# Performance work log

Hardware: AMD Instinct MI355X
Metric: run time of the kernel (lower is better)

## Reference

```python
import jax, jax.numpy as jnp
import numpy as np

NUM_EMBEDDINGS = 1024
EMBEDDING_DIM = 256


def setup_inputs() -> dict:
    key = jax.random.key(0)
    kx, kw = jax.random.split(key)
    x = jax.random.normal(kx, (64, 32, 32, EMBEDDING_DIM), dtype=jnp.float32)
    # nn.Linear(embedding_dim, num_embeddings).weight has shape [K, D]
    W = jax.random.normal(kw, (NUM_EMBEDDINGS, EMBEDDING_DIM), dtype=jnp.float32) * (1.0 / np.sqrt(EMBEDDING_DIM))
    return {"x": x, "W": W}


def reference(x, W):
    # flatten tokens: [N, D]
    flat = x.reshape(-1, EMBEDDING_DIM)
    sim = flat @ W.T
    distances = (jnp.sum(flat * flat, axis=1, keepdims=True)
                 + jnp.sum(W * W, axis=1)
                 - 2.0 * sim)
    indices = jnp.argmin(distances, axis=1)[:, None]  # [N, 1], matches torch unsqueeze(1)
    # one-hot @ W is exactly a row gather of the codebook
    quantized = jnp.take(W, indices[:, 0], axis=0).reshape(x.shape)
    return quantized, indices
```

## Files before the change

### kernel.cpp

```cpp
#include <hip/hip_runtime.h>
#include <float.h>

typedef _Float16 half8  __attribute__((ext_vector_type(8)));
typedef __fp16   fp16x2 __attribute__((ext_vector_type(2)));
typedef float    f32x4  __attribute__((ext_vector_type(4)));

#define NTOK  65536
#define DIM   256
#define NCODE 1024
#define TT    64
#define NCT   16
#define CAP   4096
#define TAU   0.08f
#define BIAS  64.0f

__device__ inline half8 pack8(float4 a, float4 b) {
    union { half8 v; fp16x2 h[4]; } u;
    u.h[0] = __builtin_amdgcn_cvt_pkrtz(a.x, a.y);
    u.h[1] = __builtin_amdgcn_cvt_pkrtz(a.z, a.w);
    u.h[2] = __builtin_amdgcn_cvt_pkrtz(b.x, b.y);
    u.h[3] = __builtin_amdgcn_cvt_pkrtz(b.z, b.w);
    return u.v;
}
__device__ inline unsigned umn(unsigned a, unsigned b) { return a < b ? a : b; }
__device__ inline unsigned umx(unsigned a, unsigned b) { return a > b ? a : b; }

__device__ inline void gload16(const void* g, void* l) {
    __builtin_amdgcn_global_load_lds(
        (__attribute__((address_space(1))) void*)(size_t)g,
        (__attribute__((address_space(3))) void*)l,
        16, 0, 0);
}

__global__ __launch_bounds__(256) void prep_kernel(const float* __restrict__ W,
                                                   float* __restrict__ nw_out,
                                                   half8* __restrict__ wh_out) {
    const int tid = threadIdx.x;
    const int k = blockIdx.x * 8 + (tid >> 5);
    const int c = tid & 31;
    const float4* wr = (const float4*)(W + (size_t)k * DIM + c * 8);
    float4 u = wr[0], v = wr[1];
    wh_out[(size_t)k * 32 + c] = pack8(u, v);
    double a = (double)u.x * u.x + (double)u.y * u.y + (double)u.z * u.z + (double)u.w * u.w
             + (double)v.x * v.x + (double)v.y * v.y + (double)v.z * v.z + (double)v.w * v.w;
    #pragma unroll
    for (int m = 1; m <= 16; m <<= 1) a += __shfl_xor(a, m);
    if (c == 0) nw_out[k] = (float)a;
}

template <bool PRE>
__global__ __launch_bounds__(256) __attribute__((amdgpu_waves_per_eu(4, 4)))
void vq_kernel(
    const float* __restrict__ x, const float* __restrict__ W,
    const float* __restrict__ nwp, const half8* __restrict__ whp,
    float* __restrict__ outq, float* __restrict__ outidx)
{
    __shared__ _Float16 wtile[64][256];
    __shared__ float nw_s[NCODE];
    __shared__ float nx_s[TT];
    __shared__ unsigned long long best64[TT];
    __shared__ int cnt_s;
    __shared__ int bk_s[TT];
    unsigned* cand = (unsigned*)&wtile[0][0];

    const int tid = threadIdx.x, tb = blockIdx.x * TT;
    const int wv = tid >> 6, l = tid & 63;
    const int lg = l >> 4;
    const int lr = l & 15;

    if (PRE) {
        ((float4*)nw_s)[tid] = ((const float4*)nwp)[tid];
    } else {
        #pragma unroll
        for (int c = 0; c < 4; ++c) {
            const int k = (tid << 2) + c;
            const float4* wr = (const float4*)(W + (size_t)k * DIM);
            double a0 = 0.0, a1 = 0.0;
            for (int q = 0; q < DIM / 4; ++q) {
                float4 v = wr[q];
                a0 += (double)v.x * v.x + (double)v.y * v.y;
                a1 += (double)v.z * v.z + (double)v.w * v.w;
            }
            nw_s[k] = (float)(a0 + a1);
        }
    }
    if (tid == 0) cnt_s = 0;
    if (tid < TT) best64[tid] = ~0ull;

    const int trow = tb + (wv << 4) + lr;
    half8 xa[8];
    {
        double a0 = 0.0, a1 = 0.0;
        #pragma unroll
        for (int s = 0; s < 8; ++s) {
            const float4* p = (const float4*)(x + (size_t)trow * DIM + (s << 5) + (lg << 3));
            float4 u = p[0], v = p[1];
            xa[s] = pack8(u, v);
            a0 += (double)u.x * u.x + (double)u.y * u.y + (double)v.x * v.x + (double)v.y * v.y;
            a1 += (double)u.z * u.z + (double)u.w * u.w + (double)v.z * v.z + (double)v.w * v.w;
        }
        double nx = a0 + a1;
        nx += __shfl_xor(nx, 16);
        nx += __shfl_xor(nx, 32);
        if (lg == 0) nx_s[(wv << 4) + lr] = (float)nx;
    }

    unsigned srcoff[8];
    #pragma unroll
    for (int j = 0; j < 8; ++j) {
        const unsigned g = (unsigned)(j * 256 + tid);
        srcoff[j] = (g & ~31u) | ((g & 31u) ^ ((g >> 5) & 31u));
    }

    unsigned b0[4], b1[4];
    #pragma unroll
    for (int j = 0; j < 4; ++j) { b0[j] = 0xFFFFFFFFu; b1[j] = 0xFFFFFFFFu; }

    for (int ct = 0; ct < NCT; ++ct) {
        __syncthreads();
        if (PRE) {
            #pragma unroll
            for (int j = 0; j < 8; ++j)
                gload16(whp + (size_t)ct * 2048 + srcoff[j],
                        (_Float16*)&wtile[0][0] + (size_t)(j * 256 + tid) * 8);
        } else {
            const int n = tid >> 2, qq = tid & 3;
            const float4* srcp = (const float4*)(W + (size_t)(ct * 64 + n) * DIM + (qq << 6));
            #pragma unroll
            for (int i = 0; i < 8; ++i) {
                float4 a = srcp[2 * i], b = srcp[2 * i + 1];
                const int c = (qq << 3) + i, p = c ^ (n & 31);
                *(half8*)&wtile[n][p << 3] = pack8(a, b);
            }
        }
        __syncthreads();

        f32x4 acc[4];
        #pragma unroll
        for (int st = 0; st < 4; ++st)
            #pragma unroll
            for (int j = 0; j < 4; ++j) acc[st][j] = 0.0f;

        #pragma unroll
        for (int sp = 0; sp < 8; ++sp) {
            const int c = (sp << 2) + lg;
            #pragma unroll
            for (int st = 0; st < 4; ++st) {
                const int n = (st << 4) + lr;
                const int p = c ^ (n & 31);
                half8 q = *(const half8*)&wtile[n][p << 3];
                acc[st] = __builtin_amdgcn_mfma_f32_16x16x32_f16(xa[sp], q, acc[st], 0, 0, 0);
            }
        }

        #pragma unroll
        for (int st = 0; st < 4; ++st) {
            const int kk = (ct << 6) + (st << 4) + lr;
            const float nwb = nw_s[kk] + BIAS;
            #pragma unroll
            for (int j = 0; j < 4; ++j) {
                const float c = fmaf(acc[st][j], -2.0f, nwb);
                const unsigned u = (__float_as_uint(c) & 0xFFFFFC00u) | (unsigned)kk;
                const unsigned lo = umn(u, b0[j]), hi = umx(u, b0[j]);
                b0[j] = lo;
                b1[j] = umn(hi, b1[j]);
            }
        }
    }

    __syncthreads();

    #pragma unroll
    for (int j = 0; j < 4; ++j) {
        unsigned v = b0[j];
        #pragma unroll
        for (int m = 1; m <= 8; m <<= 1) v = umn(v, (unsigned)__shfl_xor((int)v, m));
        const float thr = __uint_as_float(v & 0xFFFFFC00u) + TAU;
        const int t = (wv << 4) + (lg << 2) + j;
        if (__uint_as_float(b0[j] & 0xFFFFFC00u) <= thr) {
            int i = atomicAdd(&cnt_s, 1);
            if (i < CAP) cand[i] = ((unsigned)t << 10) | (b0[j] & 1023u);
        }
        if (__uint_as_float(b1[j] & 0xFFFFFC00u) <= thr) {
            int i = atomicAdd(&cnt_s, 1);
            if (i < CAP) cand[i] = ((unsigned)t << 10) | (b1[j] & 1023u);
        }
    }
    __syncthreads();

    const int nc = min(cnt_s, CAP);
    for (int c = wv; c < nc; c += 4) {
        const unsigned en = cand[c];
        const int t = en >> 10, k = en & 1023;
        float4 xv = ((const float4*)(x + (size_t)(tb + t) * DIM))[l];
        float4 wr = ((const float4*)(W + (size_t)k * DIM))[l];
        float s = fmaf(xv.x, wr.x, fmaf(xv.y, wr.y, fmaf(xv.z, wr.z, xv.w * wr.w)));
        #pragma unroll
        for (int m = 1; m <= 32; m <<= 1) s += __shfl_xor(s, m);
        const float dv = (nx_s[t] + nw_s[k]) - 2.0f * s;
        if (l == 0) {
            unsigned long long key = ((unsigned long long)__float_as_uint(dv) << 32) | (unsigned)k;
            atomicMin(&best64[t], key);
        }
    }
    __syncthreads();

    if (tid < TT) {
        const int bk = (int)(best64[tid] & 1023u);
        bk_s[tid] = bk;
        outidx[tb + tid] = (float)bk;
    }
    __syncthreads();

    for (int i = tid; i < TT * (DIM / 4); i += 256) {
        const int t = i >> 6, j = i & 63;
        const float4* wr = (const float4*)(W + (size_t)bk_s[t] * DIM);
        ((float4*)(outq + (size_t)(tb + t) * DIM))[j] = wr[j];
    }
}

extern "C" void kernel_launch(void* const* d_in, const int* in_sizes, int n_in,
                              void* d_out, int out_size, void* d_ws, size_t ws_size,
                              hipStream_t stream) {
    const float* x = (const float*)d_in[0];
    const float* W = (const float*)d_in[1];
    float* outq   = (float*)d_out;
    float* outidx = outq + (size_t)NTOK * DIM;

    const size_t need = 4096 + (size_t)NCODE * DIM * sizeof(_Float16);
    if (ws_size >= need) {
        float* nw_ws = (float*)d_ws;
        half8* wh_ws = (half8*)((char*)d_ws + 4096);
        prep_kernel<<<NCODE / 8, 256, 0, stream>>>(W, nw_ws, wh_ws);
        vq_kernel<true><<<NTOK / TT, 256, 0, stream>>>(x, W, nw_ws, wh_ws, outq, outidx);
    } else {
        vq_kernel<false><<<NTOK / TT, 256, 0, stream>>>(x, W, nullptr, nullptr, outq, outidx);
    }
}
```

Baseline: 159.3 us.

## Retile waves into 2x2 token-by-code MFMA blocks with shared threshold reduction

Each wave now computes two 16-token tiles against two 16-code subtiles of the shared codebook tile, instead of one token tile against four code subtiles. This halves the LDS fragment reads per MFMA, because each codebook fragment is reused across two token fragments. Each wave now sees only half of each code tile, so the per-token minimum is combined across the two code-group waves with shared-memory atomicMin before candidates are thresholded. In exchange, each x row is loaded from global memory by two waves, the x register footprint doubles, and an extra reduction pass and barrier are added.

```diff
diff --git a/kernel.cpp b/kernel.cpp
--- a/kernel.cpp
+++ b/kernel.cpp
@@ -58,6 +58,7 @@
     __shared__ _Float16 wtile[64][256];
     __shared__ float nw_s[NCODE];
     __shared__ float nx_s[TT];
+    __shared__ unsigned tmin_s[TT];
     __shared__ unsigned long long best64[TT];
     __shared__ int cnt_s;
     __shared__ int bk_s[TT];
@@ -67,6 +68,8 @@
     const int wv = tid >> 6, l = tid & 63;
     const int lg = l >> 4;
     const int lr = l & 15;
+    const int tg = wv & 1;
+    const int cg = wv >> 1;
 
     if (PRE) {
         ((float4*)nw_s)[tid] = ((const float4*)nwp)[tid];
@@ -85,44 +88,53 @@
         }
     }
     if (tid == 0) cnt_s = 0;
-    if (tid < TT) best64[tid] = ~0ull;
-
-    const int trow = tb + (wv << 4) + lr;
-    half8 xa[8];
+    if (tid < TT) { best64[tid] = ~0ull; tmin_s[tid] = 0xFFFFFFFFu; }
+
+    half8 xa0[8], xa1[8];
     {
-        double a0 = 0.0, a1 = 0.0;
-        #pragma unroll
-        for (int s = 0; s < 8; ++s) {
-            const float4* p = (const float4*)(x + (size_t)trow * DIM + (s << 5) + (lg << 3));
-            float4 u = p[0], v = p[1];
-            xa[s] = pack8(u, v);
-            a0 += (double)u.x * u.x + (double)u.y * u.y + (double)v.x * v.x + (double)v.y * v.y;
-            a1 += (double)u.z * u.z + (double)u.w * u.w + (double)v.z * v.z + (double)v.w * v.w;
-        }
-        double nx = a0 + a1;
-        nx += __shfl_xor(nx, 16);
-        nx += __shfl_xor(nx, 32);
-        if (lg == 0) nx_s[(wv << 4) + lr] = (float)nx;
-    }
-
-    unsigned srcoff[8];
-    #pragma unroll
-    for (int j = 0; j < 8; ++j) {
-        const unsigned g = (unsigned)(j * 256 + tid);
-        srcoff[j] = (g & ~31u) | ((g & 31u) ^ ((g >> 5) & 31u));
-    }
-
-    unsigned b0[4], b1[4];
-    #pragma unroll
-    for (int j = 0; j < 4; ++j) { b0[j] = 0xFFFFFFFFu; b1[j] = 0xFFFFFFFFu; }
+        const float4* p0 = (const float4*)(x + (size_t)(tb + (tg << 5) + lr) * DIM + (lg << 3));
+        const float4* p1 = (const float4*)(x + (size_t)(tb + (tg << 5) + 16 + lr) * DIM + (lg << 3));
+        double a0 = 0.0, a1 = 0.0, c0 = 0.0, c1 = 0.0;
+        #pragma unroll
+        for (int sp = 0; sp < 8; ++sp) {
+            float4 u = p0[sp * 8], v = p0[sp * 8 + 1];
+            xa0[sp] = pack8(u, v);
+            float4 uu = p1[sp * 8], vv = p1[sp * 8 + 1];
+            xa1[sp] = pack8(uu, vv);
+            if (cg == 0) {
+                a0 += (double)u.x * u.x + (double)u.y * u.y + (double)v.x * v.x + (double)v.y * v.y;
+                a1 += (double)u.z * u.z + (double)u.w * u.w + (double)v.z * v.z + (double)v.w * v.w;
+                c0 += (double)uu.x * uu.x + (double)uu.y * uu.y + (double)vv.x * vv.x + (double)vv.y * vv.y;
+                c1 += (double)uu.z * uu.z + (double)uu.w * uu.w + (double)vv.z * vv.z + (double)vv.w * vv.w;
+            }
+        }
+        if (cg == 0) {
+            double n0 = a0 + a1, n1 = c0 + c1;
+            n0 += __shfl_xor(n0, 16); n0 += __shfl_xor(n0, 32);
+            n1 += __shfl_xor(n1, 16); n1 += __shfl_xor(n1, 32);
+            if (lg == 0) {
+                nx_s[(tg << 5) + lr]      = (float)n0;
+                nx_s[(tg << 5) + 16 + lr] = (float)n1;
+            }
+        }
+    }
+
+    unsigned b0[2][4], b1[2][4];
+    #pragma unroll
+    for (int s = 0; s < 2; ++s)
+        #pragma unroll
+        for (int j = 0; j < 4; ++j) { b0[s][j] = 0xFFFFFFFFu; b1[s][j] = 0xFFFFFFFFu; }
 
     for (int ct = 0; ct < NCT; ++ct) {
         __syncthreads();
         if (PRE) {
             #pragma unroll
-            for (int j = 0; j < 8; ++j)
-                gload16(whp + (size_t)ct * 2048 + srcoff[j],
-                        (_Float16*)&wtile[0][0] + (size_t)(j * 256 + tid) * 8);
+            for (int j = 0; j < 8; ++j) {
+                const unsigned g = (unsigned)(j * 256 + tid);
+                const unsigned src = (g & ~31u) | ((g & 31u) ^ ((g >> 5) & 31u));
+                gload16(whp + (size_t)ct * 2048 + src,
+                        (_Float16*)&wtile[0][0] + (size_t)g * 8);
+            }
         } else {
             const int n = tid >> 2, qq = tid & 3;
             const float4* srcp = (const float4*)(W + (size_t)(ct * 64 + n) * DIM + (qq << 6));
@@ -135,57 +147,80 @@
         }
         __syncthreads();
 
-        f32x4 acc[4];
-        #pragma unroll
-        for (int st = 0; st < 4; ++st)
-            #pragma unroll
-            for (int j = 0; j < 4; ++j) acc[st][j] = 0.0f;
+        f32x4 a00, a01, a10, a11;
+        #pragma unroll
+        for (int j = 0; j < 4; ++j) { a00[j] = 0.f; a01[j] = 0.f; a10[j] = 0.f; a11[j] = 0.f; }
 
         #pragma unroll
         for (int sp = 0; sp < 8; ++sp) {
             const int c = (sp << 2) + lg;
+            const int n0 = (cg << 5) + lr;
+            const int n1 = n0 + 16;
+            half8 q0 = *(const half8*)&wtile[n0][(c ^ (n0 & 31)) << 3];
+            half8 q1 = *(const half8*)&wtile[n1][(c ^ (n1 & 31)) << 3];
+            a00 = __builtin_amdgcn_mfma_f32_16x16x32_f16(xa0[sp], q0, a00, 0, 0, 0);
+            a10 = __builtin_amdgcn_mfma_f32_16x16x32_f16(xa1[sp], q0, a10, 0, 0, 0);
+            a01 = __builtin_amdgcn_mfma_f32_16x16x32_f16(xa0[sp], q1, a01, 0, 0, 0);
+            a11 = __builtin_amdgcn_mfma_f32_16x16x32_f16(xa1[sp], q1, a11, 0, 0, 0);
+        }
+
+        const int kkb = (ct << 6) + (cg << 5) + lr;
+        const float nwb0 = nw_s[kkb] + BIAS;
+        const float nwb1 = nw_s[kkb + 16] + BIAS;
+        #pragma unroll
+        for (int j = 0; j < 4; ++j) {
+            {
+                const float c0 = fmaf(a00[j], -2.0f, nwb0);
+                unsigned u = (__float_as_uint(c0) & 0xFFFFFC00u) | (unsigned)kkb;
+                unsigned lo = umn(u, b0[0][j]), hi = umx(u, b0[0][j]);
+                b0[0][j] = lo; b1[0][j] = umn(hi, b1[0][j]);
+                const float c1 = fmaf(a01[j], -2.0f, nwb1);
+                u = (__float_as_uint(c1) & 0xFFFFFC00u) | (unsigned)(kkb + 16);
+                lo = umn(u, b0[0][j]); hi = umx(u, b0[0][j]);
+                b0[0][j] = lo; b1[0][j] = umn(hi, b1[0][j]);
+            }
+            {
+                const float c0 = fmaf(a10[j], -2.0f, nwb0);
+                unsigned u = (__float_as_uint(c0) & 0xFFFFFC00u) | (unsigned)kkb;
+                unsigned lo = umn(u, b0[1][j]), hi = umx(u, b0[1][j]);
+                b0[1][j] = lo; b1[1][j] = umn(hi, b1[1][j]);
+                const float c1 = fmaf(a11[j], -2.0f, nwb1);
+                u = (__float_as_uint(c1) & 0xFFFFFC00u) | (unsigned)(kkb + 16);
+                lo = umn(u, b0[1][j]); hi = umx(u, b0[1][j]);
+                b0[1][j] = lo; b1[1][j] = umn(hi, b1[1][j]);
+            }
+        }
+    }
+
+    #pragma unroll
+    for (int s = 0; s < 2; ++s)
+        #pragma unroll
+        for (int j = 0; j < 4; ++j) {
+            unsigned v = b0[s][j];
             #pragma unroll
-            for (int st = 0; st < 4; ++st) {
-                const int n = (st << 4) + lr;
-                const int p = c ^ (n & 31);
-                half8 q = *(const half8*)&wtile[n][p << 3];
-                acc[st] = __builtin_amdgcn_mfma_f32_16x16x32_f16(xa[sp], q, acc[st], 0, 0, 0);
-            }
-        }
-
-        #pragma unroll
-        for (int st = 0; st < 4; ++st) {
-            const int kk = (ct << 6) + (st << 4) + lr;
-            const float nwb = nw_s[kk] + BIAS;
-            #pragma unroll
-            for (int j = 0; j < 4; ++j) {
-                const float c = fmaf(acc[st][j], -2.0f, nwb);
-                const unsigned u = (__float_as_uint(c) & 0xFFFFFC00u) | (unsigned)kk;
-                const unsigned lo = umn(u, b0[j]), hi = umx(u, b0[j]);
-                b0[j] = lo;
-                b1[j] = umn(hi, b1[j]);
-            }
-        }
-    }
-
-    __syncthreads();
-
-    #pragma unroll
-    for (int j = 0; j < 4; ++j) {
-        unsigned v = b0[j];
-        #pragma unroll
-        for (int m = 1; m <= 8; m <<= 1) v = umn(v, (unsigned)__shfl_xor((int)v, m));
-        const float thr = __uint_as_float(v & 0xFFFFFC00u) + TAU;
-        const int t = (wv << 4) + (lg << 2) + j;
-        if (__uint_as_float(b0[j] & 0xFFFFFC00u) <= thr) {
-            int i = atomicAdd(&cnt_s, 1);
-            if (i < CAP) cand[i] = ((unsigned)t << 10) | (b0[j] & 1023u);
-        }
-        if (__uint_as_float(b1[j] & 0xFFFFFC00u) <= thr) {
-            int i = atomicAdd(&cnt_s, 1);
-            if (i < CAP) cand[i] = ((unsigned)t << 10) | (b1[j] & 1023u);
-        }
-    }
+            for (int m = 1; m <= 8; m <<= 1) v = umn(v, (unsigned)__shfl_xor((int)v, m));
+            if (lr == 0) {
+                const int t = (tg << 5) + (s << 4) + (lg << 2) + j;
+                atomicMin(&tmin_s[t], v & 0xFFFFFC00u);
+            }
+        }
+    __syncthreads();
+
+    #pragma unroll
+    for (int s = 0; s < 2; ++s)
+        #pragma unroll
+        for (int j = 0; j < 4; ++j) {
+            const int t = (tg << 5) + (s << 4) + (lg << 2) + j;
+            const float thr = __uint_as_float(tmin_s[t]) + TAU;
+            if (__uint_as_float(b0[s][j] & 0xFFFFFC00u) <= thr) {
+                int i = atomicAdd(&cnt_s, 1);
+                if (i < CAP) cand[i] = ((unsigned)t << 10) | (b0[s][j] & 1023u);
+            }
+            if (__uint_as_float(b1[s][j] & 0xFFFFFC00u) <= thr) {
+                int i = atomicAdd(&cnt_s, 1);
+                if (i < CAP) cand[i] = ((unsigned)t << 10) | (b1[s][j] & 1023u);
+            }
+        }
     __syncthreads();
 
     const int nc = min(cnt_s, CAP);
```

Measured after the change: 205.6 us. +29.0%, slower.
